# Kernel tuning notes

Hardware: AMD Instinct MI355X
Metric: run time of the kernel (lower is better)

The kernel has to match this reference:

```python
import jax, jax.numpy as jnp
import numpy as np

N = 50000
E = 1_600_000
IN_DIM = 512
H1, H2 = 2048, 2048
OUT_DIM = 512


def setup_inputs() -> dict:
    key = jax.random.key(0)
    ks = jax.random.split(key, 10)
    x = jax.random.normal(ks[0], (N, IN_DIM), dtype=jnp.float32)
    edge_weight = jax.random.uniform(ks[1], (E,), dtype=jnp.float32)
    edge_src = jax.random.randint(ks[2], (E,), 0, N, dtype=jnp.int32)
    edge_dst = jax.random.randint(ks[3], (E,), 0, N, dtype=jnp.int32)
    s = 0.02  # small init scale for numerical sanity
    W1 = jax.random.normal(ks[4], (2 * IN_DIM, H1), dtype=jnp.float32) * s
    b1 = jnp.zeros((H1,), dtype=jnp.float32)
    W2 = jax.random.normal(ks[5], (H1, H2), dtype=jnp.float32) * s
    b2 = jnp.zeros((H2,), dtype=jnp.float32)
    W3 = jax.random.normal(ks[6], (H2, OUT_DIM), dtype=jnp.float32) * s
    b3 = jnp.zeros((OUT_DIM,), dtype=jnp.float32)
    return {"x": x, "edge_weight": edge_weight, "W1": W1, "b1": b1,
            "W2": W2, "b2": b2, "W3": W3, "b3": b3,
            "edge_src": edge_src, "edge_dst": edge_dst}


def reference(x, edge_weight, W1, b1, W2, b2, W3, b3, edge_src, edge_dst):
    # SpMM: agg[i] = sum_{e: dst=i} w_e * x[src_e]   (A_norm @ x in COO form)
    msgs = edge_weight[:, None] * x[edge_src]          # (E, in_dim)
    agg = jax.ops.segment_sum(msgs, edge_dst, num_segments=N)  # (N, in_dim)
    h = jnp.concatenate([x, agg], axis=1)              # (N, 2*in_dim)
    h = jax.nn.relu(h @ W1 + b1)
    h = jax.nn.relu(h @ W2 + b2)
    return h @ W3 + b3                                 # (N, out_dim)
```

## Files before the change

### kernel.cpp

```cpp
#include <hip/hip_runtime.h>

#define NNODES 50000
#define NEDGES 1600000
#define IN_DIM 512
#define K1 1024
#define H1 2048
#define H2 2048
#define OUT_DIM 512
#define MTILES 196
#define M_PAD 50176
#define SCAN_BLOCKS 49

typedef unsigned short ushort_t;
typedef short sh8 __attribute__((ext_vector_type(8)));
typedef float f32x4 __attribute__((ext_vector_type(4)));

__device__ __forceinline__ ushort_t f2bf(float f) {
    unsigned u = __float_as_uint(f);
    unsigned r = (u + 0x7FFFu + ((u >> 16) & 1u)) >> 16;
    return (ushort_t)r;
}
__device__ __forceinline__ float bf2f(ushort_t h) {
    return __uint_as_float(((unsigned)h) << 16);
}

__global__ void zero_kernel(int* __restrict__ p, int n) {
    int i = blockIdx.x * 256 + threadIdx.x;
    if (i < n) p[i] = 0;
}

__global__ void convert_x_kernel(const float* __restrict__ x, ushort_t* __restrict__ h0) {
    int t = blockIdx.x * 256 + threadIdx.x;
    int n = t >> 7, c = t & 127;
    float4 v = ((const float4*)x)[n * 128 + c];
    ushort4 o;
    o.x = f2bf(v.x); o.y = f2bf(v.y); o.z = f2bf(v.z); o.w = f2bf(v.w);
    ((ushort4*)h0)[n * 256 + c] = o;
}

__global__ void wtrans_kernel(const float* __restrict__ W, ushort_t* __restrict__ Wt,
                              int K, int Nn) {
    __shared__ float t[32][33];
    int n0 = blockIdx.x * 32, k0 = blockIdx.y * 32;
    int tx = threadIdx.x, ty = threadIdx.y;
#pragma unroll
    for (int i = 0; i < 4; i++)
        t[ty + 8 * i][tx] = W[(size_t)(k0 + ty + 8 * i) * Nn + n0 + tx];
    __syncthreads();
#pragma unroll
    for (int i = 0; i < 4; i++)
        Wt[(size_t)(n0 + ty + 8 * i) * K + k0 + tx] = f2bf(t[tx][ty + 8 * i]);
}

__global__ void hist_kernel(const int* __restrict__ edst, int* __restrict__ counts) {
    int e = blockIdx.x * 256 + threadIdx.x;
    atomicAdd(&counts[edst[e]], 1);
}

__global__ void scan_blocks_kernel(const int* __restrict__ counts, int* __restrict__ incl,
                                   int* __restrict__ block_sums) {
    __shared__ int s[1024];
    int b = blockIdx.x, tid = threadIdx.x;
    int i = b * 1024 + tid;
    int c = (i < NNODES) ? counts[i] : 0;
    s[tid] = c;
    __syncthreads();
    for (int off = 1; off < 1024; off <<= 1) {
        int v = (tid >= off) ? s[tid - off] : 0;
        __syncthreads();
        s[tid] += v;
        __syncthreads();
    }
    if (i < NNODES) incl[i] = s[tid];
    if (tid == 1023) block_sums[b] = s[1023];
}

__global__ void scan_sums_kernel(const int* __restrict__ block_sums, int* __restrict__ carry) {
    if (threadIdx.x == 0 && blockIdx.x == 0) {
        int run = 0;
        for (int b = 0; b < SCAN_BLOCKS; b++) { carry[b] = run; run += block_sums[b]; }
    }
}

__global__ void scan_finalize_kernel(const int* __restrict__ counts, const int* __restrict__ incl,
                                     const int* __restrict__ carry, int* __restrict__ offsets,
                                     int* __restrict__ cursor) {
    int b = blockIdx.x, tid = threadIdx.x;
    int i = b * 1024 + tid;
    if (i < NNODES) {
        int v = incl[i] + carry[b];
        offsets[i + 1] = v;
        cursor[i] = v - counts[i];
    }
    if (i == 0) offsets[0] = 0;
}

__global__ void scatter_kernel(const int* __restrict__ edst, int* __restrict__ cursor,
                               int* __restrict__ perm) {
    int e = blockIdx.x * 256 + threadIdx.x;
    int d = edst[e];
    int pos = atomicAdd(&cursor[d], 1);
    perm[pos] = e;
}

__global__ void aggregate_kernel(ushort_t* __restrict__ h0,
                                 const float* __restrict__ ew,
                                 const int* __restrict__ esrc,
                                 const int* __restrict__ offsets,
                                 const int* __restrict__ perm) {
    __shared__ int se[128];
    __shared__ float swt[128];
    int n = blockIdx.x;
    int tid = threadIdx.x;
    int beg = offsets[n], end = offsets[n + 1];
    float a0 = 0.f, a1 = 0.f, a2 = 0.f, a3 = 0.f;
    for (int base = beg; base < end; base += 128) {
        int cnt = end - base; if (cnt > 128) cnt = 128;
        if (tid < cnt) {
            int e = perm[base + tid];
            se[tid] = esrc[e];
            swt[tid] = ew[e];
        }
        __syncthreads();
        int j = 0;
        for (; j + 8 <= cnt; j += 8) {
            ushort4 v[8]; float w[8];
#pragma unroll
            for (int u = 0; u < 8; u++) {
                int s = se[j + u];
                w[u] = swt[j + u];
                v[u] = *(const ushort4*)&h0[(size_t)s * 1024 + tid * 4];
            }
#pragma unroll
            for (int u = 0; u < 8; u++) {
                a0 += w[u] * bf2f(v[u].x);
                a1 += w[u] * bf2f(v[u].y);
                a2 += w[u] * bf2f(v[u].z);
                a3 += w[u] * bf2f(v[u].w);
            }
        }
        for (; j < cnt; j++) {
            int s = se[j];
            float w = swt[j];
            ushort4 v = *(const ushort4*)&h0[(size_t)s * 1024 + tid * 4];
            a0 += w * bf2f(v.x);
            a1 += w * bf2f(v.y);
            a2 += w * bf2f(v.z);
            a3 += w * bf2f(v.w);
        }
        __syncthreads();
    }
    ushort4 o;
    o.x = f2bf(a0); o.y = f2bf(a1); o.z = f2bf(a2); o.w = f2bf(a3);
    *(ushort4*)&h0[(size_t)n * 1024 + 512 + tid * 4] = o;
}

#define BAR() do { __builtin_amdgcn_sched_barrier(0); __builtin_amdgcn_s_barrier(); \
                   __builtin_amdgcn_sched_barrier(0); } while (0)

#define STAGE(MAT, HALF, T, D) do {                                                      \
    _Pragma("unroll")                                                                    \
    for (int j = 0; j < 2; j++) {                                                        \
        const ushort_t* src = ((MAT) ? pb[j] : pa[j]) + (size_t)(HALF) * 128 * LDK + (size_t)(T) * 64; \
        __builtin_amdgcn_global_load_lds(                                                \
            (const __attribute__((address_space(1))) void*)src,                          \
            (__attribute__((address_space(3))) void*)(lds + ((MAT) * 32768u + (D) * 16384u + (HALF) * 8192u + (unsigned)(wid * 2 + j) * 512u)), \
            16, 0, 0);                                                                   \
    }                                                                                    \
} while (0)

#define LDA(DST, MH, RB) do {                                                            \
    _Pragma("unroll")                                                                    \
    for (int mq = 0; mq < 4; mq++)                                                       \
        _Pragma("unroll")                                                                \
        for (int ks = 0; ks < 2; ks++)                                                   \
            DST[mq * 2 + ks] = *(const sh8*)(aL + (RB) + ((MH) * 4 + mq) * 2048 + ks * 1024); \
} while (0)

#define LDB(DST, NH, RB) do {                                                            \
    _Pragma("unroll")                                                                    \
    for (int nq = 0; nq < 2; nq++)                                                       \
        _Pragma("unroll")                                                                \
        for (int ks = 0; ks < 2; ks++)                                                   \
            DST[nq * 2 + ks] = *(const sh8*)(bL + (RB) + ((NH) * 2 + nq) * 2048 + ks * 1024); \
} while (0)

#define MM(AF, BF, MH, NH) do {                                                          \
    __builtin_amdgcn_s_setprio(1);                                                       \
    _Pragma("unroll")                                                                    \
    for (int mq = 0; mq < 4; mq++)                                                       \
        _Pragma("unroll")                                                                \
        for (int nq = 0; nq < 2; nq++)                                                   \
            _Pragma("unroll")                                                            \
            for (int ks = 0; ks < 2; ks++)                                               \
                acc[(MH) * 4 + mq][(NH) * 2 + nq] = __builtin_amdgcn_mfma_f32_16x16x32_bf16( \
                    AF[mq * 2 + ks], BF[nq * 2 + ks], acc[(MH) * 4 + mq][(NH) * 2 + nq], 0, 0, 0); \
    __builtin_amdgcn_s_setprio(0);                                                       \
} while (0)

#define TILE(T, D) do {                                                                  \
    LDA(af0, 0, (D) * 32768); LDB(bf0, 0, (D) * 32768);                                  \
    if ((T) + 1 < NT) STAGE(0, 0, (T) + 1, (D) ^ 1);                                     \
    BAR(); MM(af0, bf0, 0, 0); BAR();                                                    \
    LDB(bf1, 1, (D) * 32768);                                                            \
    if ((T) + 1 < NT) STAGE(0, 1, (T) + 1, (D) ^ 1);                                     \
    BAR(); MM(af0, bf1, 0, 1); BAR();                                                    \
    LDA(af1, 1, (D) * 32768);                                                            \
    if ((T) + 2 < NT) STAGE(1, 0, (T) + 2, (D));                                         \
    BAR(); MM(af1, bf1, 1, 1); BAR();                                                    \
    if ((T) + 2 < NT) {                                                                  \
        STAGE(1, 1, (T) + 2, (D));                                                       \
        asm volatile("s_waitcnt vmcnt(4)" ::: "memory");                                 \
    } else {                                                                             \
        asm volatile("s_waitcnt vmcnt(0)" ::: "memory");                                 \
    }                                                                                    \
    BAR(); MM(af1, bf0, 1, 0); BAR();                                                    \
} while (0)

template <int LDK, int KLEN, int NOUT, bool RELU, int OUTMODE>
__launch_bounds__(512, 2)
__global__ void gemm256(const ushort_t* __restrict__ A, const ushort_t* __restrict__ B,
                        const float* __restrict__ bias, void* __restrict__ C, int Mvalid) {
    __shared__ __align__(16) ushort_t lds[65536];
    const int tid = threadIdx.x;
    const int wid = tid >> 6, lane = tid & 63;
    const int lrow = lane & 15, lq = lane >> 4;
    const int wm = wid >> 2, wn = wid & 3;
    const int m0 = blockIdx.y * 256, n0 = blockIdx.x * 256;
    const int NT = KLEN / 64;
    const int koff = (OUTMODE == 2) ? blockIdx.z * KLEN : 0;

    const ushort_t* pa[2];
    const ushort_t* pb[2];
#pragma unroll
    for (int j = 0; j < 2; j++) {
        int p = (wid * 2 + j) * 1024 + lane * 16;
        int q = p ^ (((p >> 9) & 1) << 5);
        int row = ((q >> 11) << 4) | ((q >> 6) & 15);
        int k   = (((q >> 10) & 1) << 5) | ((q & 63) >> 1);
        pa[j] = A + (size_t)(m0 + row) * LDK + k + koff;
        pb[j] = B + (size_t)(n0 + row) * LDK + k + koff;
    }

    const int abase = (lrow * 64 + lq * 16) ^ ((lrow & 8) << 2);
    const char* aL = (const char*)lds + wm * 16384 + abase;
    const char* bL = (const char*)lds + 65536 + (wn >> 1) * 16384 + (wn & 1) * 8192 + abase;

    f32x4 acc[8][4] = {};
    sh8 af0[8], af1[8], bf0[4], bf1[4];

    STAGE(0, 0, 0, 0); STAGE(0, 1, 0, 0); STAGE(1, 0, 0, 0); STAGE(1, 1, 0, 0);
    STAGE(1, 0, 1, 1); STAGE(1, 1, 1, 1);
    asm volatile("s_waitcnt vmcnt(4)" ::: "memory");
    BAR();

#pragma unroll 1
    for (int t = 0; t < NT; t += 2) {
        TILE(t, 0);
        TILE(t + 1, 1);
    }

    int gcol[4]; float bv[4];
#pragma unroll
    for (int nn = 0; nn < 4; nn++) {
        gcol[nn] = n0 + wn * 64 + nn * 16 + lrow;
        bv[nn] = (OUTMODE != 2 || blockIdx.z == 0) ? bias[gcol[nn]] : 0.f;
    }
#pragma unroll
    for (int mm = 0; mm < 8; mm++) {
#pragma unroll
        for (int r = 0; r < 4; r++) {
            int gm = m0 + wm * 128 + mm * 16 + lq * 4 + r;
#pragma unroll
            for (int nn = 0; nn < 4; nn++) {
                float v = acc[mm][nn][r] + bv[nn];
                if (RELU) v = v > 0.f ? v : 0.f;
                if (OUTMODE == 1) {
                    ((ushort_t*)C)[(size_t)gm * NOUT + gcol[nn]] = f2bf(v);
                } else if (OUTMODE == 0) {
                    if (gm < Mvalid) ((float*)C)[(size_t)gm * NOUT + gcol[nn]] = v;
                } else {
                    if (gm < Mvalid) atomicAdd(&((float*)C)[(size_t)gm * NOUT + gcol[nn]], v);
                }
            }
        }
    }
}

static inline size_t align256(size_t x) { return (x + 255) & ~(size_t)255; }

extern "C" void kernel_launch(void* const* d_in, const int* in_sizes, int n_in,
                              void* d_out, int out_size, void* d_ws, size_t ws_size,
                              hipStream_t stream) {
    const float* x   = (const float*)d_in[0];
    const float* ew  = (const float*)d_in[1];
    const float* W1  = (const float*)d_in[2];
    const float* b1  = (const float*)d_in[3];
    const float* W2  = (const float*)d_in[4];
    const float* b2  = (const float*)d_in[5];
    const float* W3  = (const float*)d_in[6];
    const float* b3  = (const float*)d_in[7];
    const int* esrc  = (const int*)d_in[8];
    const int* edst  = (const int*)d_in[9];
    float* out = (float*)d_out;

    char* ws = (char*)d_ws;
    size_t off = 0;
    ushort_t* h0  = (ushort_t*)(ws + off); off = align256(off + (size_t)M_PAD * 1024 * 2);
    ushort_t* w1t = (ushort_t*)(ws + off); off = align256(off + (size_t)H1 * K1 * 2);
    ushort_t* w2t = (ushort_t*)(ws + off); off = align256(off + (size_t)H2 * H1 * 2);
    ushort_t* w3t = (ushort_t*)(ws + off); off = align256(off + (size_t)OUT_DIM * H2 * 2);
    size_t fixed_end = off;

    const size_t per_tile = (size_t)256 * 2048 * 2 * 2;
    size_t avail = (ws_size > fixed_end + 512) ? (ws_size - fixed_end - 512) : 0;
    int T = (int)(avail / per_tile);
    if (T > MTILES) T = MTILES;
    if (T < 4) T = 4;
    int nchunks = (MTILES + T - 1) / T;
    T = (MTILES + nchunks - 1) / nchunks;

    ushort_t* h1c = (ushort_t*)(ws + fixed_end);
    ushort_t* h2c = (ushort_t*)(ws + fixed_end + (size_t)T * 256 * 2048 * 2);

    size_t coff = fixed_end;
    int* counts     = (int*)(ws + coff); coff = align256(coff + (size_t)NNODES * 4);
    int* offsets    = (int*)(ws + coff); coff = align256(coff + (size_t)(NNODES + 1) * 4);
    int* cursor     = (int*)(ws + coff); coff = align256(coff + (size_t)NNODES * 4);
    int* incl       = (int*)(ws + coff); coff = align256(coff + (size_t)NNODES * 4);
    int* perm       = (int*)(ws + coff); coff = align256(coff + (size_t)NEDGES * 4);
    int* block_sums = (int*)(ws + coff); coff = align256(coff + (size_t)SCAN_BLOCKS * 4);
    int* carry      = (int*)(ws + coff); coff = align256(coff + (size_t)SCAN_BLOCKS * 4);

    zero_kernel<<<(NNODES + 255) / 256, 256, 0, stream>>>(counts, NNODES);
    zero_kernel<<<(NNODES * OUT_DIM + 255) / 256, 256, 0, stream>>>((int*)out, NNODES * OUT_DIM);

    convert_x_kernel<<<25000, 256, 0, stream>>>(x, h0);

    zero_kernel<<<(90112 + 255) / 256, 256, 0, stream>>>((int*)(h0 + (size_t)NNODES * 1024), 90112);

    wtrans_kernel<<<dim3(H1 / 32, K1 / 32), dim3(32, 8), 0, stream>>>(W1, w1t, K1, H1);
    wtrans_kernel<<<dim3(H2 / 32, H1 / 32), dim3(32, 8), 0, stream>>>(W2, w2t, H1, H2);
    wtrans_kernel<<<dim3(OUT_DIM / 32, H2 / 32), dim3(32, 8), 0, stream>>>(W3, w3t, H2, OUT_DIM);

    hist_kernel<<<NEDGES / 256, 256, 0, stream>>>(edst, counts);
    scan_blocks_kernel<<<SCAN_BLOCKS, 1024, 0, stream>>>(counts, incl, block_sums);
    scan_sums_kernel<<<1, 64, 0, stream>>>(block_sums, carry);
    scan_finalize_kernel<<<SCAN_BLOCKS, 1024, 0, stream>>>(counts, incl, carry, offsets, cursor);
    scatter_kernel<<<NEDGES / 256, 256, 0, stream>>>(edst, cursor, perm);

    aggregate_kernel<<<NNODES, 128, 0, stream>>>(h0, ew, esrc, offsets, perm);

    for (int t0 = 0; t0 < MTILES; t0 += T) {
        int tiles = MTILES - t0; if (tiles > T) tiles = T;
        int row0 = t0 * 256;
        gemm256<K1, K1, H1, true, 1><<<dim3(H1 / 256, tiles), 512, 0, stream>>>(
            h0 + (size_t)row0 * K1, w1t, b1, h1c, 0);
        gemm256<H1, H1, H2, true, 1><<<dim3(H2 / 256, tiles), 512, 0, stream>>>(
            h1c, w2t, b2, h2c, 0);
        gemm256<H2, 512, OUT_DIM, false, 2><<<dim3(OUT_DIM / 256, tiles, 4), 512, 0, stream>>>(
            h2c, w3t, b3, out + (size_t)row0 * OUT_DIM, NNODES - row0);
    }
}
```

Measured before the change: 1.822 ms.

## Replace atomic split-K in final GEMM with two-way partial buffer and combine

The last GEMM used to split K four ways and accumulate into a zeroed output with float atomics. It now splits two ways: z=0 writes straight to the output with bias, z=1 writes into a scratch buffer that reuses h1c, and a small combine kernel adds the two. This removes the output zeroing pass and the atomic read-modify-write traffic, at the cost of an extra kernel and a partial-buffer round trip. Workgroup IDs are also remapped so consecutive tiles land on the same XCD, which should improve L2 reuse.

```diff
diff --git a/kernel.cpp b/kernel.cpp
--- a/kernel.cpp
+++ b/kernel.cpp
@@ -155,6 +155,18 @@
     *(ushort4*)&h0[(size_t)n * 1024 + 512 + tid * 4] = o;
 }
 
+__global__ void combine_kernel(float* __restrict__ out, const float* __restrict__ p,
+                               int n4, int mvalid) {
+    int i = blockIdx.x * 256 + threadIdx.x;
+    if (i >= n4) return;
+    int row = i >> 7;
+    if (row >= mvalid) return;
+    float4 a = ((float4*)out)[i];
+    float4 b = ((const float4*)p)[i];
+    a.x += b.x; a.y += b.y; a.z += b.z; a.w += b.w;
+    ((float4*)out)[i] = a;
+}
+
 #define BAR() do { __builtin_amdgcn_sched_barrier(0); __builtin_amdgcn_s_barrier(); \
                    __builtin_amdgcn_sched_barrier(0); } while (0)
 
@@ -220,24 +232,35 @@
 template <int LDK, int KLEN, int NOUT, bool RELU, int OUTMODE>
 __launch_bounds__(512, 2)
 __global__ void gemm256(const ushort_t* __restrict__ A, const ushort_t* __restrict__ B,
-                        const float* __restrict__ bias, void* __restrict__ C, int Mvalid) {
+                        const float* __restrict__ bias, void* __restrict__ C,
+                        float* __restrict__ P, int Mvalid) {
     __shared__ __align__(16) ushort_t lds[65536];
     const int tid = threadIdx.x;
     const int wid = tid >> 6, lane = tid & 63;
     const int lrow = lane & 15, lq = lane >> 4;
     const int wm = wid >> 2, wn = wid & 3;
-    const int m0 = blockIdx.y * 256, n0 = blockIdx.x * 256;
     const int NT = KLEN / 64;
-    const int koff = (OUTMODE == 2) ? blockIdx.z * KLEN : 0;
+    const int koff = (OUTMODE == 3) ? blockIdx.z * KLEN : 0;
+
+    const int NBX = gridDim.x;
+    const int nwg = NBX * gridDim.y;
+    {
+    }
+    int L = blockIdx.y * NBX + blockIdx.x;
+    int q = nwg >> 3, r = nwg & 7;
+    int xcd = L & 7, idx = L >> 3;
+    int wgid = (xcd < r ? xcd * (q + 1) : r * (q + 1) + (xcd - r) * q) + idx;
+    const int m0 = (wgid / NBX) * 256;
+    const int n0 = (wgid % NBX) * 256;
 
     const ushort_t* pa[2];
     const ushort_t* pb[2];
 #pragma unroll
     for (int j = 0; j < 2; j++) {
         int p = (wid * 2 + j) * 1024 + lane * 16;
-        int q = p ^ (((p >> 9) & 1) << 5);
-        int row = ((q >> 11) << 4) | ((q >> 6) & 15);
-        int k   = (((q >> 10) & 1) << 5) | ((q & 63) >> 1);
+        int qq = p ^ (((p >> 9) & 1) << 5);
+        int row = ((qq >> 11) << 4) | ((qq >> 6) & 15);
+        int k   = (((qq >> 10) & 1) << 5) | ((qq & 63) >> 1);
         pa[j] = A + (size_t)(m0 + row) * LDK + k + koff;
         pb[j] = B + (size_t)(n0 + row) * LDK + k + koff;
     }
@@ -261,26 +284,26 @@
     }
 
     int gcol[4]; float bv[4];
+    const bool addbias = (OUTMODE != 3) || (blockIdx.z == 0);
 #pragma unroll
     for (int nn = 0; nn < 4; nn++) {
         gcol[nn] = n0 + wn * 64 + nn * 16 + lrow;
-        bv[nn] = (OUTMODE != 2 || blockIdx.z == 0) ? bias[gcol[nn]] : 0.f;
-    }
+        bv[nn] = addbias ? bias[gcol[nn]] : 0.f;
+    }
+    float* fdst = (OUTMODE == 3 && blockIdx.z != 0) ? P : (float*)C;
 #pragma unroll
     for (int mm = 0; mm < 8; mm++) {
 #pragma unroll
-        for (int r = 0; r < 4; r++) {
-            int gm = m0 + wm * 128 + mm * 16 + lq * 4 + r;
+        for (int r2 = 0; r2 < 4; r2++) {
+            int gm = m0 + wm * 128 + mm * 16 + lq * 4 + r2;
 #pragma unroll
             for (int nn = 0; nn < 4; nn++) {
-                float v = acc[mm][nn][r] + bv[nn];
+                float v = acc[mm][nn][r2] + bv[nn];
                 if (RELU) v = v > 0.f ? v : 0.f;
                 if (OUTMODE == 1) {
                     ((ushort_t*)C)[(size_t)gm * NOUT + gcol[nn]] = f2bf(v);
-                } else if (OUTMODE == 0) {
-                    if (gm < Mvalid) ((float*)C)[(size_t)gm * NOUT + gcol[nn]] = v;
                 } else {
-                    if (gm < Mvalid) atomicAdd(&((float*)C)[(size_t)gm * NOUT + gcol[nn]], v);
+                    if (gm < Mvalid) fdst[(size_t)gm * NOUT + gcol[nn]] = v;
                 }
             }
         }
@@ -333,7 +356,6 @@
     int* carry      = (int*)(ws + coff); coff = align256(coff + (size_t)SCAN_BLOCKS * 4);
 
     zero_kernel<<<(NNODES + 255) / 256, 256, 0, stream>>>(counts, NNODES);
-    zero_kernel<<<(NNODES * OUT_DIM + 255) / 256, 256, 0, stream>>>((int*)out, NNODES * OUT_DIM);
 
     convert_x_kernel<<<25000, 256, 0, stream>>>(x, h0);
 
@@ -355,10 +377,13 @@
         int tiles = MTILES - t0; if (tiles > T) tiles = T;
         int row0 = t0 * 256;
         gemm256<K1, K1, H1, true, 1><<<dim3(H1 / 256, tiles), 512, 0, stream>>>(
-            h0 + (size_t)row0 * K1, w1t, b1, h1c, 0);
+            h0 + (size_t)row0 * K1, w1t, b1, h1c, nullptr, 0);
         gemm256<H1, H1, H2, true, 1><<<dim3(H2 / 256, tiles), 512, 0, stream>>>(
-            h1c, w2t, b2, h2c, 0);
-        gemm256<H2, 512, OUT_DIM, false, 2><<<dim3(OUT_DIM / 256, tiles, 4), 512, 0, stream>>>(
-            h2c, w3t, b3, out + (size_t)row0 * OUT_DIM, NNODES - row0);
-    }
-}
+            h1c, w2t, b2, h2c, nullptr, 0);
+        gemm256<H2, 1024, OUT_DIM, false, 3><<<dim3(OUT_DIM / 256, tiles, 2), 512, 0, stream>>>(
+            h2c, w3t, b3, out + (size_t)row0 * OUT_DIM, (float*)h1c, NNODES - row0);
+        combine_kernel<<<(tiles * 256 * OUT_DIM / 4 + 255) / 256, 256, 0, stream>>>(
+            out + (size_t)row0 * OUT_DIM, (const float*)h1c,
+            tiles * 256 * OUT_DIM / 4, NNODES - row0);
+    }
+}
```

Measured after the change: 1.574 ms. 1.16x faster.

## Replace split-K atomic layer-3 GEMM with 256x128 tile kernel, drop output zeroing

Applied to the files above, without the earlier changes.

The final GEMM (2048->512) used to be split four ways along K, with each split writing its partial results to the output through float atomicAdd, and the output had to be zeroed first. A new 256x128-tile kernel with a 64x32 per-wave layout and a smaller LDS footprint now runs the whole K dimension and stores results directly. This removes the atomic traffic and the memset of the output buffer. The cost is a smaller grid in that stage (4 column tiles instead of 2x4 splits per M tile) and lower MFMA density per B load.

```diff
diff --git a/kernel.cpp b/kernel.cpp
--- a/kernel.cpp
+++ b/kernel.cpp
@@ -217,7 +217,7 @@
     BAR(); MM(af1, bf0, 1, 0); BAR();                                                    \
 } while (0)
 
-template <int LDK, int KLEN, int NOUT, bool RELU, int OUTMODE>
+template <int LDK, int NOUT, bool RELU, bool OUTBF16>
 __launch_bounds__(512, 2)
 __global__ void gemm256(const ushort_t* __restrict__ A, const ushort_t* __restrict__ B,
                         const float* __restrict__ bias, void* __restrict__ C, int Mvalid) {
@@ -227,8 +227,7 @@
     const int lrow = lane & 15, lq = lane >> 4;
     const int wm = wid >> 2, wn = wid & 3;
     const int m0 = blockIdx.y * 256, n0 = blockIdx.x * 256;
-    const int NT = KLEN / 64;
-    const int koff = (OUTMODE == 2) ? blockIdx.z * KLEN : 0;
+    const int NT = LDK / 64;
 
     const ushort_t* pa[2];
     const ushort_t* pb[2];
@@ -238,8 +237,8 @@
         int q = p ^ (((p >> 9) & 1) << 5);
         int row = ((q >> 11) << 4) | ((q >> 6) & 15);
         int k   = (((q >> 10) & 1) << 5) | ((q & 63) >> 1);
-        pa[j] = A + (size_t)(m0 + row) * LDK + k + koff;
-        pb[j] = B + (size_t)(n0 + row) * LDK + k + koff;
+        pa[j] = A + (size_t)(m0 + row) * LDK + k;
+        pb[j] = B + (size_t)(n0 + row) * LDK + k;
     }
 
     const int abase = (lrow * 64 + lq * 16) ^ ((lrow & 8) << 2);
@@ -264,7 +263,7 @@
 #pragma unroll
     for (int nn = 0; nn < 4; nn++) {
         gcol[nn] = n0 + wn * 64 + nn * 16 + lrow;
-        bv[nn] = (OUTMODE != 2 || blockIdx.z == 0) ? bias[gcol[nn]] : 0.f;
+        bv[nn] = bias[gcol[nn]];
     }
 #pragma unroll
     for (int mm = 0; mm < 8; mm++) {
@@ -275,13 +274,130 @@
             for (int nn = 0; nn < 4; nn++) {
                 float v = acc[mm][nn][r] + bv[nn];
                 if (RELU) v = v > 0.f ? v : 0.f;
-                if (OUTMODE == 1) {
+                if (OUTBF16) {
                     ((ushort_t*)C)[(size_t)gm * NOUT + gcol[nn]] = f2bf(v);
-                } else if (OUTMODE == 0) {
+                } else {
                     if (gm < Mvalid) ((float*)C)[(size_t)gm * NOUT + gcol[nn]] = v;
-                } else {
-                    if (gm < Mvalid) atomicAdd(&((float*)C)[(size_t)gm * NOUT + gcol[nn]], v);
                 }
+            }
+        }
+    }
+}
+
+#define STAGE_AN(HALF, T, D) do {                                                        \
+    _Pragma("unroll")                                                                    \
+    for (int j = 0; j < 2; j++) {                                                        \
+        const ushort_t* src = pa[j] + (size_t)(HALF) * 128 * LDK + (size_t)(T) * 64;     \
+        __builtin_amdgcn_global_load_lds(                                                \
+            (const __attribute__((address_space(1))) void*)src,                          \
+            (__attribute__((address_space(3))) void*)(lds + ((D) * 16384u + (HALF) * 8192u + (unsigned)(wid * 2 + j) * 512u)), \
+            16, 0, 0);                                                                   \
+    }                                                                                    \
+} while (0)
+
+#define STAGE_BN(T, D) do {                                                              \
+    _Pragma("unroll")                                                                    \
+    for (int j = 0; j < 2; j++) {                                                        \
+        const ushort_t* src = pb[j] + (size_t)(T) * 64;                                  \
+        __builtin_amdgcn_global_load_lds(                                                \
+            (const __attribute__((address_space(1))) void*)src,                          \
+            (__attribute__((address_space(3))) void*)(lds + (32768u + (D) * 8192u + (unsigned)(wid * 2 + j) * 512u)), \
+            16, 0, 0);                                                                   \
+    }                                                                                    \
+} while (0)
+
+#define LDB4(D) do {                                                                     \
+    _Pragma("unroll")                                                                    \
+    for (int nq = 0; nq < 2; nq++)                                                       \
+        _Pragma("unroll")                                                                \
+        for (int ks = 0; ks < 2; ks++)                                                   \
+            bf[nq * 2 + ks] = *(const sh8*)(bL + (D) * 16384 + nq * 2048 + ks * 1024);   \
+} while (0)
+
+#define MMN(AF, MH) do {                                                                 \
+    __builtin_amdgcn_s_setprio(1);                                                       \
+    _Pragma("unroll")                                                                    \
+    for (int mq = 0; mq < 4; mq++)                                                       \
+        _Pragma("unroll")                                                                \
+        for (int nq = 0; nq < 2; nq++)                                                   \
+            _Pragma("unroll")                                                            \
+            for (int ks = 0; ks < 2; ks++)                                               \
+                acc[(MH) * 4 + mq][nq] = __builtin_amdgcn_mfma_f32_16x16x32_bf16(        \
+                    AF[mq * 2 + ks], bf[nq * 2 + ks], acc[(MH) * 4 + mq][nq], 0, 0, 0);  \
+    __builtin_amdgcn_s_setprio(0);                                                       \
+} while (0)
+
+#define TILEN(T, D) do {                                                                 \
+    LDA(af0, 0, (D) * 32768); LDB4(D);                                                   \
+    if ((T) + 1 < NT) STAGE_AN(1, (T) + 1, (D) ^ 1);                                     \
+    BAR(); MMN(af0, 0); BAR();                                                           \
+    LDA(af1, 1, (D) * 32768);                                                            \
+    if ((T) + 2 < NT) {                                                                  \
+        STAGE_AN(0, (T) + 2, (D)); STAGE_BN((T) + 2, (D));                               \
+        asm volatile("s_waitcnt vmcnt(4)" ::: "memory");                                 \
+    } else {                                                                             \
+        asm volatile("s_waitcnt vmcnt(0)" ::: "memory");                                 \
+    }                                                                                    \
+    BAR(); MMN(af1, 1); BAR();                                                           \
+} while (0)
+
+template <int LDK, int NOUT>
+__launch_bounds__(512, 2)
+__global__ void gemm256n128(const ushort_t* __restrict__ A, const ushort_t* __restrict__ B,
+                            const float* __restrict__ bias, float* __restrict__ C, int Mvalid) {
+    __shared__ __align__(16) ushort_t lds[49152];
+    const int tid = threadIdx.x;
+    const int wid = tid >> 6, lane = tid & 63;
+    const int lrow = lane & 15, lq = lane >> 4;
+    const int wm = wid >> 2, wn = wid & 3;
+    const int m0 = blockIdx.y * 256, n0 = blockIdx.x * 128;
+    const int NT = LDK / 64;
+
+    const ushort_t* pa[2];
+    const ushort_t* pb[2];
+#pragma unroll
+    for (int j = 0; j < 2; j++) {
+        int p = (wid * 2 + j) * 1024 + lane * 16;
+        int q = p ^ (((p >> 9) & 1) << 5);
+        int row = ((q >> 11) << 4) | ((q >> 6) & 15);
+        int k   = (((q >> 10) & 1) << 5) | ((q & 63) >> 1);
+        pa[j] = A + (size_t)(m0 + row) * LDK + k;
+        pb[j] = B + (size_t)(n0 + row) * LDK + k;
+    }
+
+    const int abase = (lrow * 64 + lq * 16) ^ ((lrow & 8) << 2);
+    const char* aL = (const char*)lds + wm * 16384 + abase;
+    const char* bL = (const char*)lds + 65536 + wn * 4096 + abase;
+
+    f32x4 acc[8][2] = {};
+    sh8 af0[8], af1[8], bf[4];
+
+    STAGE_AN(0, 0, 0); STAGE_AN(1, 0, 0); STAGE_BN(0, 0);
+    STAGE_AN(0, 1, 1); STAGE_BN(1, 1);
+    asm volatile("s_waitcnt vmcnt(4)" ::: "memory");
+    BAR();
+
+#pragma unroll 1
+    for (int t = 0; t < NT; t += 2) {
+        TILEN(t, 0);
+        TILEN(t + 1, 1);
+    }
+
+    int gcol[2]; float bv[2];
+#pragma unroll
+    for (int nq = 0; nq < 2; nq++) {
+        gcol[nq] = n0 + wn * 32 + nq * 16 + lrow;
+        bv[nq] = bias[gcol[nq]];
+    }
+#pragma unroll
+    for (int mm = 0; mm < 8; mm++) {
+#pragma unroll
+        for (int r = 0; r < 4; r++) {
+            int gm = m0 + wm * 128 + mm * 16 + lq * 4 + r;
+            if (gm < Mvalid) {
+#pragma unroll
+                for (int nq = 0; nq < 2; nq++)
+                    C[(size_t)gm * NOUT + gcol[nq]] = acc[mm][nq][r] + bv[nq];
             }
         }
     }
@@ -333,7 +449,6 @@
     int* carry      = (int*)(ws + coff); coff = align256(coff + (size_t)SCAN_BLOCKS * 4);
 
     zero_kernel<<<(NNODES + 255) / 256, 256, 0, stream>>>(counts, NNODES);
-    zero_kernel<<<(NNODES * OUT_DIM + 255) / 256, 256, 0, stream>>>((int*)out, NNODES * OUT_DIM);
 
     convert_x_kernel<<<25000, 256, 0, stream>>>(x, h0);
 
@@ -354,11 +469,11 @@
     for (int t0 = 0; t0 < MTILES; t0 += T) {
         int tiles = MTILES - t0; if (tiles > T) tiles = T;
         int row0 = t0 * 256;
-        gemm256<K1, K1, H1, true, 1><<<dim3(H1 / 256, tiles), 512, 0, stream>>>(
+        gemm256<K1, H1, true, true><<<dim3(H1 / 256, tiles), 512, 0, stream>>>(
             h0 + (size_t)row0 * K1, w1t, b1, h1c, 0);
-        gemm256<H1, H1, H2, true, 1><<<dim3(H2 / 256, tiles), 512, 0, stream>>>(
+        gemm256<H1, H2, true, true><<<dim3(H2 / 256, tiles), 512, 0, stream>>>(
             h1c, w2t, b2, h2c, 0);
-        gemm256<H2, 512, OUT_DIM, false, 2><<<dim3(OUT_DIM / 256, tiles, 4), 512, 0, stream>>>(
+        gemm256n128<H2, OUT_DIM><<<dim3(OUT_DIM / 128, tiles), 512, 0, stream>>>(
             h2c, w3t, b3, out + (size_t)row0 * OUT_DIM, NNODES - row0);
     }
 }
```

New measurement: 1.558 ms. -14.5%, faster.
